# Kernel optimization log

Measured on AMD Instinct MI355X. Metric: run time of the kernel, lower is better.

## Reference

```python
import jax, jax.numpy as jnp
import numpy as np

D_MODEL = 1024
D_FF = 4096
N_EXPERTS = 8
K_ACTIVE = 2
LB_WEIGHT = 0.01
B, K = 8, 2048


def setup_inputs() -> dict:
    key = jax.random.key(0)
    ks = jax.random.split(key, 6)
    s_in = 1.0 / np.sqrt(D_MODEL)
    s_ff = 1.0 / np.sqrt(D_FF)
    return {
        "x": jax.random.normal(ks[0], (B, K, D_MODEL), dtype=jnp.float32),
        "w_router": jax.random.uniform(ks[1], (D_MODEL, N_EXPERTS), jnp.float32, -s_in, s_in),
        "W1": jax.random.uniform(ks[2], (N_EXPERTS, D_MODEL, D_FF), jnp.float32, -s_in, s_in),
        "b1": jax.random.uniform(ks[3], (N_EXPERTS, D_FF), jnp.float32, -s_in, s_in),
        "W2": jax.random.uniform(ks[4], (N_EXPERTS, D_FF, D_MODEL), jnp.float32, -s_ff, s_ff),
        "b2": jax.random.uniform(ks[5], (N_EXPERTS, D_MODEL), jnp.float32, -s_ff, s_ff),
    }


def reference(x, w_router, W1, b1, W2, b2):
    Bb, Kk, D = x.shape
    xf = x.reshape(Bb * Kk, D)                      # (T, D)
    logits = xf @ w_router                          # (T, E)
    probs = jax.nn.softmax(logits, axis=-1)
    topk_p, topk_i = jax.lax.top_k(probs, K_ACTIVE)  # (T, k)
    topk_p = topk_p / topk_p.sum(axis=-1, keepdims=True)
    oh = jax.nn.one_hot(topk_i, N_EXPERTS, dtype=xf.dtype)   # (T, k, E)
    w = (oh * topk_p[..., None]).sum(axis=1)        # (T, E) combine weights, 0 if not routed
    out = jnp.zeros_like(xf)
    for e in range(N_EXPERTS):
        h = jax.nn.gelu(xf @ W1[e] + b1[e], approximate=False)  # exact GELU as torch default
        y = h @ W2[e] + b2[e]
        out = out + w[:, e:e + 1] * y               # zero weight == token not routed to e
    f = oh.mean(axis=(0, 1))                        # fraction of (token,slot) pairs per expert
    P = probs.mean(axis=0)
    aux_loss = N_EXPERTS * (f * P).sum() * LB_WEIGHT
    return out.reshape(Bb, Kk, D), aux_loss
```

## Files before the change

kernel.cpp:

```cpp
#include <hip/hip_runtime.h>
#include <cstdint>

#define T_TOK   16384
#define DM      1024
#define DFF     4096
#define NE      8

typedef unsigned short u16;
typedef __bf16 bf16x8 __attribute__((ext_vector_type(8)));
typedef float  f32x4  __attribute__((ext_vector_type(4)));

__device__ __forceinline__ u16 f2bf(float f) {
  unsigned u = __float_as_uint(f);
  u = u + 0x7FFFu + ((u >> 16) & 1u);
  return (u16)(u >> 16);
}

__device__ __forceinline__ void async_copy16(void* lds, const void* g) {
  __builtin_amdgcn_global_load_lds(
      (const __attribute__((address_space(1))) unsigned int*)g,
      (__attribute__((address_space(3))) unsigned int*)lds, 16, 0, 0);
}

__global__ __launch_bounds__(256) void convert_x_kernel(
    const float* __restrict__ x, u16* __restrict__ xb) {
  int i = blockIdx.x * 256 + threadIdx.x;
  float4 v = ((const float4*)x)[i];
  uint2 o;
  o.x = (unsigned)f2bf(v.x) | ((unsigned)f2bf(v.y) << 16);
  o.y = (unsigned)f2bf(v.z) | ((unsigned)f2bf(v.w) << 16);
  ((uint2*)xb)[i] = o;
}

__global__ __launch_bounds__(256) void transpose_convert_kernel(
    const float* __restrict__ in, u16* __restrict__ out, int R, int C) {
  __shared__ float tile[32][33];
  int e = blockIdx.z;
  int r0 = blockIdx.y * 32, c0 = blockIdx.x * 32;
  int tx = threadIdx.x, ty = threadIdx.y;
  const float* src = in + (size_t)e * R * C;
  u16* dst = out + (size_t)e * R * C;
  #pragma unroll
  for (int i = 0; i < 32; i += 8)
    tile[ty + i][tx] = src[(size_t)(r0 + ty + i) * C + (c0 + tx)];
  __syncthreads();
  #pragma unroll
  for (int i = 0; i < 32; i += 8)
    dst[(size_t)(c0 + ty + i) * R + (r0 + tx)] = f2bf(tile[tx][ty + i]);
}

__global__ __launch_bounds__(256) void router_kernel(
    const float* __restrict__ x, const float* __restrict__ wr,
    int* __restrict__ tok_e, float* __restrict__ tok_w,
    int* __restrict__ counts, float* __restrict__ psum) {
  __shared__ float ps[NE];
  __shared__ int   pc[NE];
  int tid = threadIdx.x, wave = tid >> 6, lane = tid & 63;
  if (tid < NE) { ps[tid] = 0.f; pc[tid] = 0; }
  __syncthreads();

  int t = blockIdx.x * 4 + wave;
  const float* xrow = x + (size_t)t * DM;
  float acc[NE];
  #pragma unroll
  for (int e = 0; e < NE; ++e) acc[e] = 0.f;
  for (int j = 0; j < DM / 64; ++j) {
    float xv = xrow[j * 64 + lane];
    const float* w = wr + (size_t)(j * 64 + lane) * NE;
    #pragma unroll
    for (int e = 0; e < NE; ++e) acc[e] += xv * w[e];
  }
  #pragma unroll
  for (int m = 1; m < 64; m <<= 1) {
    #pragma unroll
    for (int e = 0; e < NE; ++e) acc[e] += __shfl_xor(acc[e], m, 64);
  }
  if (lane == 0) {
    float mx = acc[0];
    #pragma unroll
    for (int e = 1; e < NE; ++e) mx = fmaxf(mx, acc[e]);
    float p[NE], s = 0.f;
    #pragma unroll
    for (int e = 0; e < NE; ++e) { p[e] = expf(acc[e] - mx); s += p[e]; }
    float inv = 1.f / s;
    int i1 = 0; float b1v = p[0];
    #pragma unroll
    for (int e = 1; e < NE; ++e) if (p[e] > b1v) { b1v = p[e]; i1 = e; }
    int i2 = -1; float b2v = -1.f;
    #pragma unroll
    for (int e = 0; e < NE; ++e) if (e != i1 && p[e] > b2v) { b2v = p[e]; i2 = e; }
    float wsum = b1v + b2v;
    tok_e[2 * t]     = i1;  tok_e[2 * t + 1] = i2;
    tok_w[2 * t]     = b1v / wsum;
    tok_w[2 * t + 1] = b2v / wsum;
    atomicAdd(&pc[i1], 1); atomicAdd(&pc[i2], 1);
    #pragma unroll
    for (int e = 0; e < NE; ++e) atomicAdd(&ps[e], p[e] * inv);
  }
  __syncthreads();
  if (tid < NE) { atomicAdd(&counts[tid], pc[tid]); atomicAdd(&psum[tid], ps[tid]); }
}

__global__ void scan_kernel(const int* __restrict__ counts, int* __restrict__ offsets) {
  if (threadIdx.x == 0) {
    int r = 0;
    for (int e = 0; e < NE; ++e) { offsets[e] = r; r += counts[e]; }
  }
}

__global__ __launch_bounds__(256) void build_lists_kernel(
    const int* __restrict__ tok_e, const float* __restrict__ tok_w,
    const int* __restrict__ offsets, int* __restrict__ fill,
    int* __restrict__ rowlist, float* __restrict__ roww) {
  int t = blockIdx.x * 256 + threadIdx.x;
  #pragma unroll
  for (int s = 0; s < 2; ++s) {
    int e = tok_e[2 * t + s];
    int pos = atomicAdd(&fill[e], 1);
    int idx = offsets[e] + pos;
    rowlist[idx] = t;
    roww[idx] = tok_w[2 * t + s];
  }
}

template <int PASS>
__global__ __launch_bounds__(256) void moe_gemm_kernel(
    const u16* __restrict__ Asrc, const u16* __restrict__ BT,
    const float* __restrict__ bias,
    const int* __restrict__ counts, const int* __restrict__ offsets,
    const int* __restrict__ rowlist, const float* __restrict__ roww,
    u16* __restrict__ Hout, float* __restrict__ Out) {
  constexpr int K = (PASS == 1) ? DM : DFF;
  constexpr int N = (PASS == 1) ? DFF : DM;

  const int e = blockIdx.z;
  const int cnt = counts[e];
  const int row0 = blockIdx.y * 128;
  if (row0 >= cnt) return;
  const int off = offsets[e];
  const int nb = blockIdx.x * 128;
  const int tid = threadIdx.x, wave = tid >> 6, lane = tid & 63;

  __shared__ u16 lsA[128 * 64];
  __shared__ u16 lsB[128 * 64];

  const int sw = (((lane & 7) ^ (lane >> 3)) * 8);
  const u16* aPtr[4];
  const u16* bPtr[4];
  #pragma unroll
  for (int i = 0; i < 4; ++i) {
    int rowi = (wave * 4 + i) * 8 + (lane >> 3);
    int r = row0 + rowi;
    int rr = (r < cnt) ? r : (cnt - 1);
    int srcrow;
    if (PASS == 1) srcrow = rowlist[off + rr];
    else           srcrow = off + rr;
    aPtr[i] = Asrc + (size_t)srcrow * K + sw;
    bPtr[i] = BT + ((size_t)e * N + (nb + rowi)) * K + sw;
  }

  f32x4 acc[4][4];
  #pragma unroll
  for (int m = 0; m < 4; ++m)
    #pragma unroll
    for (int n = 0; n < 4; ++n) acc[m][n] = (f32x4){0.f, 0.f, 0.f, 0.f};

  const int wm = wave >> 1, wn = wave & 1;

  for (int kt = 0; kt < K; kt += 64) {
    #pragma unroll
    for (int i = 0; i < 4; ++i) {
      async_copy16(&lsA[(wave * 4 + i) * 512], aPtr[i] + kt);
      async_copy16(&lsB[(wave * 4 + i) * 512], bPtr[i] + kt);
    }
    __syncthreads();
    #pragma unroll
    for (int ks = 0; ks < 2; ++ks) {
      const int cbase = (((ks * 4 + (lane >> 4)) ^ (lane & 7)) * 8);
      bf16x8 af[4], bfr[4];
      #pragma unroll
      for (int m = 0; m < 4; ++m) {
        int rowA = wm * 64 + m * 16 + (lane & 15);
        af[m] = *(const bf16x8*)&lsA[rowA * 64 + cbase];
      }
      #pragma unroll
      for (int n = 0; n < 4; ++n) {
        int rowB = wn * 64 + n * 16 + (lane & 15);
        bfr[n] = *(const bf16x8*)&lsB[rowB * 64 + cbase];
      }
      #pragma unroll
      for (int m = 0; m < 4; ++m)
        #pragma unroll
        for (int n = 0; n < 4; ++n)
          acc[m][n] = __builtin_amdgcn_mfma_f32_16x16x32_bf16(af[m], bfr[n], acc[m][n], 0, 0, 0);
    }
    __syncthreads();
  }

  float bv[4];
  #pragma unroll
  for (int n = 0; n < 4; ++n)
    bv[n] = bias[e * N + nb + wn * 64 + n * 16 + (lane & 15)];

  if (PASS == 1) {
    #pragma unroll
    for (int m = 0; m < 4; ++m) {
      #pragma unroll
      for (int j = 0; j < 4; ++j) {
        int r = row0 + wm * 64 + m * 16 + (lane >> 4) * 4 + j;
        if (r < cnt) {
          size_t base = (size_t)(off + r) * DFF;
          #pragma unroll
          for (int n = 0; n < 4; ++n) {
            int c = nb + wn * 64 + n * 16 + (lane & 15);
            float v = acc[m][n][j] + bv[n];
            v = 0.5f * v * (1.f + erff(v * 0.70710678118654752f));
            Hout[base + c] = f2bf(v);
          }
        }
      }
    }
  } else {
    #pragma unroll
    for (int m = 0; m < 4; ++m) {
      #pragma unroll
      for (int j = 0; j < 4; ++j) {
        int r = row0 + wm * 64 + m * 16 + (lane >> 4) * 4 + j;
        if (r < cnt) {
          int t = rowlist[off + r];
          float w = roww[off + r];
          size_t base = (size_t)t * DM;
          #pragma unroll
          for (int n = 0; n < 4; ++n) {
            int c = nb + wn * 64 + n * 16 + (lane & 15);
            atomicAdd(&Out[base + c], w * (acc[m][n][j] + bv[n]));
          }
        }
      }
    }
  }
}

__global__ void aux_kernel(const int* __restrict__ counts, const float* __restrict__ psum,
                           float* __restrict__ out_aux) {
  if (threadIdx.x == 0) {
    float s = 0.f;
    for (int e = 0; e < NE; ++e)
      s += ((float)counts[e] / (float)(2 * T_TOK)) * (psum[e] / (float)T_TOK);
    *out_aux = (float)NE * 0.01f * s;
  }
}

extern "C" void kernel_launch(void* const* d_in, const int* in_sizes, int n_in,
                              void* d_out, int out_size, void* d_ws, size_t ws_size,
                              hipStream_t stream) {
  const float* x  = (const float*)d_in[0];
  const float* wr = (const float*)d_in[1];
  const float* W1 = (const float*)d_in[2];
  const float* b1 = (const float*)d_in[3];
  const float* W2 = (const float*)d_in[4];
  const float* b2 = (const float*)d_in[5];
  float* out = (float*)d_out;
  char* ws = (char*)d_ws;

  int*   counts  = (int*)(ws + 0);
  int*   fill    = (int*)(ws + 32);
  float* psum    = (float*)(ws + 64);
  int*   offsets = (int*)(ws + 96);
  int*   tok_e   = (int*)(ws + 256);
  float* tok_w   = (float*)(ws + 256 + 131072);
  int*   rowlist = (int*)(ws + 256 + 2 * 131072);
  float* roww    = (float*)(ws + 256 + 3 * 131072);
  const size_t MiB = 1ull << 20;
  u16* xb  = (u16*)(ws + 1 * MiB);
  u16* W1T = (u16*)(ws + 33 * MiB);
  u16* W2T = (u16*)(ws + 97 * MiB);
  u16* h   = (u16*)(ws + 161 * MiB);

  hipMemsetAsync(ws, 0, 256, stream);
  hipMemsetAsync(d_out, 0, (size_t)out_size * sizeof(float), stream);

  convert_x_kernel<<<T_TOK * DM / 4 / 256, 256, 0, stream>>>(x, xb);
  transpose_convert_kernel<<<dim3(DFF / 32, DM / 32, NE), dim3(32, 8), 0, stream>>>(W1, W1T, DM, DFF);
  transpose_convert_kernel<<<dim3(DM / 32, DFF / 32, NE), dim3(32, 8), 0, stream>>>(W2, W2T, DFF, DM);
  router_kernel<<<T_TOK / 4, 256, 0, stream>>>(x, wr, tok_e, tok_w, counts, psum);
  scan_kernel<<<1, 64, 0, stream>>>(counts, offsets);
  build_lists_kernel<<<T_TOK / 256, 256, 0, stream>>>(tok_e, tok_w, offsets, fill, rowlist, roww);
  moe_gemm_kernel<1><<<dim3(DFF / 128, T_TOK / 128, NE), 256, 0, stream>>>(
      xb, W1T, b1, counts, offsets, rowlist, roww, h, nullptr);
  moe_gemm_kernel<2><<<dim3(DM / 128, T_TOK / 128, NE), 256, 0, stream>>>(
      h, W2T, b2, counts, offsets, rowlist, roww, nullptr, out);
  aux_kernel<<<1, 64, 0, stream>>>(counts, psum, out + (size_t)T_TOK * DM);
}
```

Before: 1.628 ms.

## Swap GEMM operand roles for vector stores, add polynomial GELU and atomic-free combine

Swaps the MFMA operand order so each lane's accumulator holds four consecutive output columns, which allows vectorized 8-byte bf16 stores of H and float4 stores of Y. Replaces erff with an Abramowitz-Stegun polynomial erf that uses a fast reciprocal and exp. When the workspace is large enough, the second GEMM writes per-slot outputs to a buffer and a separate combine kernel gathers each token's two rows, so the float atomics and the output memset are no longer needed. The cost is an extra 64 MiB intermediate round trip, and the new GELU is less accurate than erff.

```diff
diff --git a/kernel.cpp b/kernel.cpp
--- a/kernel.cpp
+++ b/kernel.cpp
@@ -9,11 +9,27 @@
 typedef unsigned short u16;
 typedef __bf16 bf16x8 __attribute__((ext_vector_type(8)));
 typedef float  f32x4  __attribute__((ext_vector_type(4)));
+typedef u16    u16x4  __attribute__((ext_vector_type(4)));
 
 __device__ __forceinline__ u16 f2bf(float f) {
   unsigned u = __float_as_uint(f);
   u = u + 0x7FFFu + ((u >> 16) & 1u);
   return (u16)(u >> 16);
+}
+
+__device__ __forceinline__ float gelu_exact(float v) {
+  float x  = v * 0.70710678118654752f;
+  float ax = fabsf(x);
+  float t  = __builtin_amdgcn_rcpf(fmaf(0.3275911f, ax, 1.0f));
+  float p  = fmaf(1.061405429f, t, -1.453152027f);
+  p = fmaf(p, t, 1.421413741f);
+  p = fmaf(p, t, -0.284496736f);
+  p = fmaf(p, t, 0.254829592f);
+  p = p * t;
+  float e  = __expf(-x * x);
+  float er = fmaf(-p, e, 1.0f);
+  er = copysignf(er, x);
+  return 0.5f * v * (1.0f + er);
 }
 
 __device__ __forceinline__ void async_copy16(void* lds, const void* g) {
@@ -111,7 +127,7 @@
 __global__ __launch_bounds__(256) void build_lists_kernel(
     const int* __restrict__ tok_e, const float* __restrict__ tok_w,
     const int* __restrict__ offsets, int* __restrict__ fill,
-    int* __restrict__ rowlist, float* __restrict__ roww) {
+    int* __restrict__ rowlist, float* __restrict__ roww, int* __restrict__ spos) {
   int t = blockIdx.x * 256 + threadIdx.x;
   #pragma unroll
   for (int s = 0; s < 2; ++s) {
@@ -120,16 +136,17 @@
     int idx = offsets[e] + pos;
     rowlist[idx] = t;
     roww[idx] = tok_w[2 * t + s];
-  }
-}
-
-template <int PASS>
+    spos[2 * t + s] = idx;
+  }
+}
+
+template <int PASS, bool ATOMIC>
 __global__ __launch_bounds__(256) void moe_gemm_kernel(
     const u16* __restrict__ Asrc, const u16* __restrict__ BT,
     const float* __restrict__ bias,
     const int* __restrict__ counts, const int* __restrict__ offsets,
     const int* __restrict__ rowlist, const float* __restrict__ roww,
-    u16* __restrict__ Hout, float* __restrict__ Out) {
+    u16* __restrict__ Hout, float* __restrict__ Yout, float* __restrict__ Out) {
   constexpr int K = (PASS == 1) ? DM : DFF;
   constexpr int N = (PASS == 1) ? DFF : DM;
 
@@ -161,11 +178,11 @@
 
   f32x4 acc[4][4];
   #pragma unroll
-  for (int m = 0; m < 4; ++m)
-    #pragma unroll
-    for (int n = 0; n < 4; ++n) acc[m][n] = (f32x4){0.f, 0.f, 0.f, 0.f};
-
-  const int wm = wave >> 1, wn = wave & 1;
+  for (int p = 0; p < 4; ++p)
+    #pragma unroll
+    for (int q = 0; q < 4; ++q) acc[p][q] = (f32x4){0.f, 0.f, 0.f, 0.f};
+
+  const int wu = wave >> 1, wv = wave & 1;
 
   for (int kt = 0; kt < K; kt += 64) {
     #pragma unroll
@@ -177,68 +194,96 @@
     #pragma unroll
     for (int ks = 0; ks < 2; ++ks) {
       const int cbase = (((ks * 4 + (lane >> 4)) ^ (lane & 7)) * 8);
-      bf16x8 af[4], bfr[4];
-      #pragma unroll
-      for (int m = 0; m < 4; ++m) {
-        int rowA = wm * 64 + m * 16 + (lane & 15);
-        af[m] = *(const bf16x8*)&lsA[rowA * 64 + cbase];
-      }
-      #pragma unroll
-      for (int n = 0; n < 4; ++n) {
-        int rowB = wn * 64 + n * 16 + (lane & 15);
-        bfr[n] = *(const bf16x8*)&lsB[rowB * 64 + cbase];
-      }
-      #pragma unroll
-      for (int m = 0; m < 4; ++m)
+      bf16x8 wf[4], xf[4];
+      #pragma unroll
+      for (int p = 0; p < 4; ++p) {
+        int rowW = wu * 64 + p * 16 + (lane & 15);
+        wf[p] = *(const bf16x8*)&lsB[rowW * 64 + cbase];
+      }
+      #pragma unroll
+      for (int q = 0; q < 4; ++q) {
+        int rowX = wv * 64 + q * 16 + (lane & 15);
+        xf[q] = *(const bf16x8*)&lsA[rowX * 64 + cbase];
+      }
+      #pragma unroll
+      for (int p = 0; p < 4; ++p)
         #pragma unroll
-        for (int n = 0; n < 4; ++n)
-          acc[m][n] = __builtin_amdgcn_mfma_f32_16x16x32_bf16(af[m], bfr[n], acc[m][n], 0, 0, 0);
+        for (int q = 0; q < 4; ++q)
+          acc[p][q] = __builtin_amdgcn_mfma_f32_16x16x32_bf16(wf[p], xf[q], acc[p][q], 0, 0, 0);
     }
     __syncthreads();
   }
 
-  float bv[4];
-  #pragma unroll
-  for (int n = 0; n < 4; ++n)
-    bv[n] = bias[e * N + nb + wn * 64 + n * 16 + (lane & 15)];
-
   if (PASS == 1) {
     #pragma unroll
-    for (int m = 0; m < 4; ++m) {
-      #pragma unroll
-      for (int j = 0; j < 4; ++j) {
-        int r = row0 + wm * 64 + m * 16 + (lane >> 4) * 4 + j;
-        if (r < cnt) {
-          size_t base = (size_t)(off + r) * DFF;
-          #pragma unroll
-          for (int n = 0; n < 4; ++n) {
-            int c = nb + wn * 64 + n * 16 + (lane & 15);
-            float v = acc[m][n][j] + bv[n];
-            v = 0.5f * v * (1.f + erff(v * 0.70710678118654752f));
-            Hout[base + c] = f2bf(v);
-          }
+    for (int p = 0; p < 4; ++p) {
+      const int ub = nb + wu * 64 + p * 16 + ((lane >> 4) << 2);
+      const float4 bv = *(const float4*)&bias[e * N + ub];
+      #pragma unroll
+      for (int q = 0; q < 4; ++q) {
+        int v = row0 + wv * 64 + q * 16 + (lane & 15);
+        if (v < cnt) {
+          u16x4 o;
+          o[0] = f2bf(gelu_exact(acc[p][q][0] + bv.x));
+          o[1] = f2bf(gelu_exact(acc[p][q][1] + bv.y));
+          o[2] = f2bf(gelu_exact(acc[p][q][2] + bv.z));
+          o[3] = f2bf(gelu_exact(acc[p][q][3] + bv.w));
+          *(u16x4*)&Hout[(size_t)(off + v) * DFF + ub] = o;
         }
       }
     }
+  } else if (!ATOMIC) {
+    #pragma unroll
+    for (int p = 0; p < 4; ++p) {
+      const int ub = nb + wu * 64 + p * 16 + ((lane >> 4) << 2);
+      #pragma unroll
+      for (int q = 0; q < 4; ++q) {
+        int v = row0 + wv * 64 + q * 16 + (lane & 15);
+        if (v < cnt)
+          *(f32x4*)&Yout[(size_t)(off + v) * DM + ub] = acc[p][q];
+      }
+    }
   } else {
     #pragma unroll
-    for (int m = 0; m < 4; ++m) {
-      #pragma unroll
-      for (int j = 0; j < 4; ++j) {
-        int r = row0 + wm * 64 + m * 16 + (lane >> 4) * 4 + j;
-        if (r < cnt) {
-          int t = rowlist[off + r];
-          float w = roww[off + r];
-          size_t base = (size_t)t * DM;
-          #pragma unroll
-          for (int n = 0; n < 4; ++n) {
-            int c = nb + wn * 64 + n * 16 + (lane & 15);
-            atomicAdd(&Out[base + c], w * (acc[m][n][j] + bv[n]));
-          }
+    for (int p = 0; p < 4; ++p) {
+      const int ub = nb + wu * 64 + p * 16 + ((lane >> 4) << 2);
+      const float4 bv = *(const float4*)&bias[e * N + ub];
+      #pragma unroll
+      for (int q = 0; q < 4; ++q) {
+        int v = row0 + wv * 64 + q * 16 + (lane & 15);
+        if (v < cnt) {
+          int t = rowlist[off + v];
+          float w = roww[off + v];
+          size_t base = (size_t)t * DM + ub;
+          atomicAdd(&Out[base + 0], w * (acc[p][q][0] + bv.x));
+          atomicAdd(&Out[base + 1], w * (acc[p][q][1] + bv.y));
+          atomicAdd(&Out[base + 2], w * (acc[p][q][2] + bv.z));
+          atomicAdd(&Out[base + 3], w * (acc[p][q][3] + bv.w));
         }
       }
     }
   }
+}
+
+__global__ __launch_bounds__(256) void combine_kernel(
+    const float* __restrict__ y, const int* __restrict__ spos,
+    const int* __restrict__ tok_e, const float* __restrict__ tok_w,
+    const float* __restrict__ b2, float* __restrict__ out) {
+  int t = blockIdx.x;
+  int c = threadIdx.x * 4;
+  int p0 = spos[2 * t], p1 = spos[2 * t + 1];
+  int e0 = tok_e[2 * t], e1 = tok_e[2 * t + 1];
+  float w0 = tok_w[2 * t], w1 = tok_w[2 * t + 1];
+  float4 a  = *(const float4*)&y[(size_t)p0 * DM + c];
+  float4 b  = *(const float4*)&y[(size_t)p1 * DM + c];
+  float4 ba = *(const float4*)&b2[e0 * DM + c];
+  float4 bb = *(const float4*)&b2[e1 * DM + c];
+  float4 o;
+  o.x = w0 * (a.x + ba.x) + w1 * (b.x + bb.x);
+  o.y = w0 * (a.y + ba.y) + w1 * (b.y + bb.y);
+  o.z = w0 * (a.z + ba.z) + w1 * (b.z + bb.z);
+  o.w = w0 * (a.w + ba.w) + w1 * (b.w + bb.w);
+  *(float4*)&out[(size_t)t * DM + c] = o;
 }
 
 __global__ void aux_kernel(const int* __restrict__ counts, const float* __restrict__ psum,
@@ -264,31 +309,42 @@
   char* ws = (char*)d_ws;
 
   int*   counts  = (int*)(ws + 0);
-  int*   fill    = (int*)(ws + 32);
-  float* psum    = (float*)(ws + 64);
-  int*   offsets = (int*)(ws + 96);
+  int*   fill    = (int*)(ws + 64);
+  float* psum    = (float*)(ws + 128);
+  int*   offsets = (int*)(ws + 192);
   int*   tok_e   = (int*)(ws + 256);
   float* tok_w   = (float*)(ws + 256 + 131072);
   int*   rowlist = (int*)(ws + 256 + 2 * 131072);
   float* roww    = (float*)(ws + 256 + 3 * 131072);
+  int*   spos    = (int*)(ws + 256 + 4 * 131072);
   const size_t MiB = 1ull << 20;
   u16* xb  = (u16*)(ws + 1 * MiB);
   u16* W1T = (u16*)(ws + 33 * MiB);
   u16* W2T = (u16*)(ws + 97 * MiB);
   u16* h   = (u16*)(ws + 161 * MiB);
+  float* y = (float*)(ws + 417 * MiB);
+
+  const bool bigws = ws_size >= (size_t)545 * MiB;
 
   hipMemsetAsync(ws, 0, 256, stream);
-  hipMemsetAsync(d_out, 0, (size_t)out_size * sizeof(float), stream);
+  if (!bigws)
+    hipMemsetAsync(d_out, 0, (size_t)out_size * sizeof(float), stream);
 
   convert_x_kernel<<<T_TOK * DM / 4 / 256, 256, 0, stream>>>(x, xb);
   transpose_convert_kernel<<<dim3(DFF / 32, DM / 32, NE), dim3(32, 8), 0, stream>>>(W1, W1T, DM, DFF);
   transpose_convert_kernel<<<dim3(DM / 32, DFF / 32, NE), dim3(32, 8), 0, stream>>>(W2, W2T, DFF, DM);
   router_kernel<<<T_TOK / 4, 256, 0, stream>>>(x, wr, tok_e, tok_w, counts, psum);
   scan_kernel<<<1, 64, 0, stream>>>(counts, offsets);
-  build_lists_kernel<<<T_TOK / 256, 256, 0, stream>>>(tok_e, tok_w, offsets, fill, rowlist, roww);
-  moe_gemm_kernel<1><<<dim3(DFF / 128, T_TOK / 128, NE), 256, 0, stream>>>(
-      xb, W1T, b1, counts, offsets, rowlist, roww, h, nullptr);
-  moe_gemm_kernel<2><<<dim3(DM / 128, T_TOK / 128, NE), 256, 0, stream>>>(
-      h, W2T, b2, counts, offsets, rowlist, roww, nullptr, out);
+  build_lists_kernel<<<T_TOK / 256, 256, 0, stream>>>(tok_e, tok_w, offsets, fill, rowlist, roww, spos);
+  moe_gemm_kernel<1, false><<<dim3(DFF / 128, T_TOK / 128, NE), 256, 0, stream>>>(
+      xb, W1T, b1, counts, offsets, rowlist, roww, h, nullptr, nullptr);
+  if (bigws) {
+    moe_gemm_kernel<2, false><<<dim3(DM / 128, T_TOK / 128, NE), 256, 0, stream>>>(
+        h, W2T, b2, counts, offsets, rowlist, roww, nullptr, y, nullptr);
+    combine_kernel<<<T_TOK, 256, 0, stream>>>(y, spos, tok_e, tok_w, b2, out);
+  } else {
+    moe_gemm_kernel<2, true><<<dim3(DM / 128, T_TOK / 128, NE), 256, 0, stream>>>(
+        h, W2T, b2, counts, offsets, rowlist, roww, nullptr, nullptr, out);
+  }
   aux_kernel<<<1, 64, 0, stream>>>(counts, psum, out + (size_t)T_TOK * DM);
 }
```

After: 1.747 ms. 1.07x slower.

## Use 256x256 double-buffered GEMM tiles with swizzled block order and fast GELU

Applied to the files above, without the earlier changes.

Both expert GEMMs move from 128x128 tiles with 256 threads to 256x256 tiles with 512 threads, and LDS is double-buffered so global-to-LDS copies overlap the MFMA work. A 1D grid is remapped across XCDs and grouped so neighbouring blocks share weight and activation tiles. The MFMA operands are swapped so each lane holds four consecutive output columns, which allows vectorized bias loads and 4-wide bf16 stores of H. erff is replaced by an Abramowitz-Stegun polynomial approximation, which adds approximation error and brings higher register and LDS pressure (acc is 4x8 per wave, 128KB LDS).

```diff
diff --git a/kernel.cpp b/kernel.cpp
--- a/kernel.cpp
+++ b/kernel.cpp
@@ -9,11 +9,27 @@
 typedef unsigned short u16;
 typedef __bf16 bf16x8 __attribute__((ext_vector_type(8)));
 typedef float  f32x4  __attribute__((ext_vector_type(4)));
+typedef u16    u16x4  __attribute__((ext_vector_type(4)));
 
 __device__ __forceinline__ u16 f2bf(float f) {
   unsigned u = __float_as_uint(f);
   u = u + 0x7FFFu + ((u >> 16) & 1u);
   return (u16)(u >> 16);
+}
+
+__device__ __forceinline__ float gelu_exact(float v) {
+  float x  = v * 0.70710678118654752f;
+  float ax = fabsf(x);
+  float t  = __builtin_amdgcn_rcpf(fmaf(0.3275911f, ax, 1.0f));
+  float p  = fmaf(1.061405429f, t, -1.453152027f);
+  p = fmaf(p, t, 1.421413741f);
+  p = fmaf(p, t, -0.284496736f);
+  p = fmaf(p, t, 0.254829592f);
+  p = p * t;
+  float e  = __expf(-x * x);
+  float er = fmaf(-p, e, 1.0f);
+  er = copysignf(er, x);
+  return 0.5f * v * (1.0f + er);
 }
 
 __device__ __forceinline__ void async_copy16(void* lds, const void* g) {
@@ -124,117 +140,127 @@
 }
 
 template <int PASS>
-__global__ __launch_bounds__(256) void moe_gemm_kernel(
+__global__ __launch_bounds__(512) void moe_gemm_kernel(
     const u16* __restrict__ Asrc, const u16* __restrict__ BT,
     const float* __restrict__ bias,
     const int* __restrict__ counts, const int* __restrict__ offsets,
     const int* __restrict__ rowlist, const float* __restrict__ roww,
     u16* __restrict__ Hout, float* __restrict__ Out) {
-  constexpr int K = (PASS == 1) ? DM : DFF;
-  constexpr int N = (PASS == 1) ? DFF : DM;
-
-  const int e = blockIdx.z;
-  const int cnt = counts[e];
-  const int row0 = blockIdx.y * 128;
+  constexpr int K   = (PASS == 1) ? DM : DFF;
+  constexpr int N   = (PASS == 1) ? DFF : DM;
+  constexpr int XB  = N / 256;
+  constexpr int SXs = XB / 4;
+  constexpr int NBLK = NE * 64 * XB;
+  constexpr int NT  = K / 64;
+
+  __shared__ u16 lsA[2][256 * 64];
+  __shared__ u16 lsB[2][256 * 64];
+
+  const int d = blockIdx.x;
+  const int w = (d & 7) * (NBLK / 8) + (d >> 3);
+  const int inner = w & 15;
+  const int sidx  = w >> 4;
+  const int e     = sidx & 7;
+  const int ss    = sidx >> 3;
+  const int sy    = ss / SXs, sx = ss % SXs;
+  const int strip = sy * 4 + (inner >> 2);
+  const int col   = sx * 4 + (inner & 3);
+
+  const int cnt  = counts[e];
+  const int row0 = strip * 256;
   if (row0 >= cnt) return;
   const int off = offsets[e];
-  const int nb = blockIdx.x * 128;
-  const int tid = threadIdx.x, wave = tid >> 6, lane = tid & 63;
-
-  __shared__ u16 lsA[128 * 64];
-  __shared__ u16 lsB[128 * 64];
-
+  const int nb  = col * 256;
+
+  const int tid = threadIdx.x, wv = tid >> 6, lane = tid & 63;
   const int sw = (((lane & 7) ^ (lane >> 3)) * 8);
+
   const u16* aPtr[4];
   const u16* bPtr[4];
   #pragma unroll
   for (int i = 0; i < 4; ++i) {
-    int rowi = (wave * 4 + i) * 8 + (lane >> 3);
+    int rowi = i * 64 + wv * 8 + (lane >> 3);
     int r = row0 + rowi;
     int rr = (r < cnt) ? r : (cnt - 1);
-    int srcrow;
-    if (PASS == 1) srcrow = rowlist[off + rr];
-    else           srcrow = off + rr;
+    int srcrow = (PASS == 1) ? rowlist[off + rr] : (off + rr);
     aPtr[i] = Asrc + (size_t)srcrow * K + sw;
     bPtr[i] = BT + ((size_t)e * N + (nb + rowi)) * K + sw;
   }
 
-  f32x4 acc[4][4];
-  #pragma unroll
-  for (int m = 0; m < 4; ++m)
-    #pragma unroll
-    for (int n = 0; n < 4; ++n) acc[m][n] = (f32x4){0.f, 0.f, 0.f, 0.f};
-
-  const int wm = wave >> 1, wn = wave & 1;
-
-  for (int kt = 0; kt < K; kt += 64) {
+  f32x4 acc[4][8];
+  #pragma unroll
+  for (int p = 0; p < 4; ++p)
+    #pragma unroll
+    for (int q = 0; q < 8; ++q) acc[p][q] = (f32x4){0.f, 0.f, 0.f, 0.f};
+
+  const int wt = wv >> 2, wq = wv & 3;
+
+  auto stage = [&](int buf, int kt) {
     #pragma unroll
     for (int i = 0; i < 4; ++i) {
-      async_copy16(&lsA[(wave * 4 + i) * 512], aPtr[i] + kt);
-      async_copy16(&lsB[(wave * 4 + i) * 512], bPtr[i] + kt);
+      async_copy16(&lsA[buf][(i * 64 + wv * 8) * 64], aPtr[i] + kt);
+      async_copy16(&lsB[buf][(i * 64 + wv * 8) * 64], bPtr[i] + kt);
     }
-    __syncthreads();
+  };
+
+  stage(0, 0);
+  __syncthreads();
+  int cur = 0;
+  for (int t = 0; t < NT; ++t) {
+    if (t + 1 < NT) stage(cur ^ 1, (t + 1) * 64);
     #pragma unroll
     for (int ks = 0; ks < 2; ++ks) {
       const int cbase = (((ks * 4 + (lane >> 4)) ^ (lane & 7)) * 8);
-      bf16x8 af[4], bfr[4];
-      #pragma unroll
-      for (int m = 0; m < 4; ++m) {
-        int rowA = wm * 64 + m * 16 + (lane & 15);
-        af[m] = *(const bf16x8*)&lsA[rowA * 64 + cbase];
-      }
-      #pragma unroll
-      for (int n = 0; n < 4; ++n) {
-        int rowB = wn * 64 + n * 16 + (lane & 15);
-        bfr[n] = *(const bf16x8*)&lsB[rowB * 64 + cbase];
-      }
-      #pragma unroll
-      for (int m = 0; m < 4; ++m)
+      bf16x8 wf[4], xf[8];
+      #pragma unroll
+      for (int p = 0; p < 4; ++p)
+        wf[p] = *(const bf16x8*)&lsB[cur][(wq * 64 + p * 16 + (lane & 15)) * 64 + cbase];
+      #pragma unroll
+      for (int q = 0; q < 8; ++q)
+        xf[q] = *(const bf16x8*)&lsA[cur][(wt * 128 + q * 16 + (lane & 15)) * 64 + cbase];
+      #pragma unroll
+      for (int p = 0; p < 4; ++p)
         #pragma unroll
-        for (int n = 0; n < 4; ++n)
-          acc[m][n] = __builtin_amdgcn_mfma_f32_16x16x32_bf16(af[m], bfr[n], acc[m][n], 0, 0, 0);
+        for (int q = 0; q < 8; ++q)
+          acc[p][q] = __builtin_amdgcn_mfma_f32_16x16x32_bf16(wf[p], xf[q], acc[p][q], 0, 0, 0);
     }
-    __syncthreads();
-  }
-
-  float bv[4];
-  #pragma unroll
-  for (int n = 0; n < 4; ++n)
-    bv[n] = bias[e * N + nb + wn * 64 + n * 16 + (lane & 15)];
+    if (t + 1 < NT) { __syncthreads(); cur ^= 1; }
+  }
 
   if (PASS == 1) {
     #pragma unroll
-    for (int m = 0; m < 4; ++m) {
-      #pragma unroll
-      for (int j = 0; j < 4; ++j) {
-        int r = row0 + wm * 64 + m * 16 + (lane >> 4) * 4 + j;
-        if (r < cnt) {
-          size_t base = (size_t)(off + r) * DFF;
-          #pragma unroll
-          for (int n = 0; n < 4; ++n) {
-            int c = nb + wn * 64 + n * 16 + (lane & 15);
-            float v = acc[m][n][j] + bv[n];
-            v = 0.5f * v * (1.f + erff(v * 0.70710678118654752f));
-            Hout[base + c] = f2bf(v);
-          }
+    for (int p = 0; p < 4; ++p) {
+      const int ub = nb + wq * 64 + p * 16 + ((lane >> 4) << 2);
+      const float4 bv = *(const float4*)&bias[e * N + ub];
+      #pragma unroll
+      for (int q = 0; q < 8; ++q) {
+        int v = row0 + wt * 128 + q * 16 + (lane & 15);
+        if (v < cnt) {
+          u16x4 o;
+          o[0] = f2bf(gelu_exact(acc[p][q][0] + bv.x));
+          o[1] = f2bf(gelu_exact(acc[p][q][1] + bv.y));
+          o[2] = f2bf(gelu_exact(acc[p][q][2] + bv.z));
+          o[3] = f2bf(gelu_exact(acc[p][q][3] + bv.w));
+          *(u16x4*)&Hout[(size_t)(off + v) * DFF + ub] = o;
         }
       }
     }
   } else {
     #pragma unroll
-    for (int m = 0; m < 4; ++m) {
-      #pragma unroll
-      for (int j = 0; j < 4; ++j) {
-        int r = row0 + wm * 64 + m * 16 + (lane >> 4) * 4 + j;
-        if (r < cnt) {
-          int t = rowlist[off + r];
-          float w = roww[off + r];
-          size_t base = (size_t)t * DM;
-          #pragma unroll
-          for (int n = 0; n < 4; ++n) {
-            int c = nb + wn * 64 + n * 16 + (lane & 15);
-            atomicAdd(&Out[base + c], w * (acc[m][n][j] + bv[n]));
-          }
+    for (int p = 0; p < 4; ++p) {
+      const int ub = nb + wq * 64 + p * 16 + ((lane >> 4) << 2);
+      const float4 bv = *(const float4*)&bias[e * N + ub];
+      #pragma unroll
+      for (int q = 0; q < 8; ++q) {
+        int v = row0 + wt * 128 + q * 16 + (lane & 15);
+        if (v < cnt) {
+          int tk = rowlist[off + v];
+          float wgt = roww[off + v];
+          size_t base = (size_t)tk * DM + ub;
+          atomicAdd(&Out[base + 0], wgt * (acc[p][q][0] + bv.x));
+          atomicAdd(&Out[base + 1], wgt * (acc[p][q][1] + bv.y));
+          atomicAdd(&Out[base + 2], wgt * (acc[p][q][2] + bv.z));
+          atomicAdd(&Out[base + 3], wgt * (acc[p][q][3] + bv.w));
         }
       }
     }
@@ -264,9 +290,9 @@
   char* ws = (char*)d_ws;
 
   int*   counts  = (int*)(ws + 0);
-  int*   fill    = (int*)(ws + 32);
-  float* psum    = (float*)(ws + 64);
-  int*   offsets = (int*)(ws + 96);
+  int*   fill    = (int*)(ws + 64);
+  float* psum    = (float*)(ws + 128);
+  int*   offsets = (int*)(ws + 192);
   int*   tok_e   = (int*)(ws + 256);
   float* tok_w   = (float*)(ws + 256 + 131072);
   int*   rowlist = (int*)(ws + 256 + 2 * 131072);
@@ -286,9 +312,9 @@
   router_kernel<<<T_TOK / 4, 256, 0, stream>>>(x, wr, tok_e, tok_w, counts, psum);
   scan_kernel<<<1, 64, 0, stream>>>(counts, offsets);
   build_lists_kernel<<<T_TOK / 256, 256, 0, stream>>>(tok_e, tok_w, offsets, fill, rowlist, roww);
-  moe_gemm_kernel<1><<<dim3(DFF / 128, T_TOK / 128, NE), 256, 0, stream>>>(
+  moe_gemm_kernel<1><<<NE * 64 * (DFF / 256), 512, 0, stream>>>(
       xb, W1T, b1, counts, offsets, rowlist, roww, h, nullptr);
-  moe_gemm_kernel<2><<<dim3(DM / 128, T_TOK / 128, NE), 256, 0, stream>>>(
+  moe_gemm_kernel<2><<<NE * 64 * (DM / 256), 512, 0, stream>>>(
       h, W2T, b2, counts, offsets, rowlist, roww, nullptr, out);
   aux_kernel<<<1, 64, 0, stream>>>(counts, psum, out + (size_t)T_TOK * DM);
 }
```

Result: slower. 3.462 ms (+112.7%).
